# Optimization experiments

Measured on AMD Instinct MI355X. Metric: run time of the kernel, lower is better.

The kernel has to match this reference:

```python
import jax, jax.numpy as jnp
import numpy as np

P = 16          # patch size
NUM_HEADS = 8
WINDOW = 64     # window_size from SparseAttention(window_size=64)


def _layer_norm(x, w, b, eps=1e-5):
    mu = jnp.mean(x, axis=-1, keepdims=True)
    var = jnp.var(x, axis=-1, keepdims=True)
    return (x - mu) * jax.lax.rsqrt(var + eps) * w + b


def _sinusoidal_pe(num_patches, num_features, dtype):
    pos = jnp.arange(num_patches, dtype=jnp.float32)[:, None]            # [N,1]
    i = jnp.arange(0, num_features, 2, dtype=jnp.float32)                # [D/2]
    div = jnp.exp(-jnp.log(10000.0) * i / num_features)                  # [D/2]
    ang = pos * div                                                      # [N,D/2]
    pe = jnp.stack([jnp.sin(ang), jnp.cos(ang)], axis=-1).reshape(num_patches, num_features)
    return pe.astype(dtype)


def _ffn(x, w1, b1, w2, b2):
    # FeedForward: Linear -> GELU -> Linear (dropout inactive at eval)
    h = jax.nn.gelu(jnp.einsum('bnd,hd->bnh', x, w1) + b1)
    return jnp.einsum('bnh,dh->bnd', h, w2) + b2


def _windowed_attention(x, qkv_w, qkv_b, proj_w, proj_b):
    B, N, D = x.shape
    hd = D // NUM_HEADS
    qkv = jnp.einsum('bnd,ed->bne', x, qkv_w) + qkv_b                    # [B,N,3D]
    qkv = qkv.reshape(B, N, 3, NUM_HEADS, hd)
    q, k, v = qkv[:, :, 0], qkv[:, :, 1], qkv[:, :, 2]                   # [B,N,H,hd]
    nw = N // WINDOW
    # partition sequence into non-overlapping windows of 64 tokens
    q = q.reshape(B, nw, WINDOW, NUM_HEADS, hd).transpose(0, 3, 1, 2, 4)  # [B,H,nw,W,hd]
    k = k.reshape(B, nw, WINDOW, NUM_HEADS, hd).transpose(0, 3, 1, 2, 4)
    v = v.reshape(B, nw, WINDOW, NUM_HEADS, hd).transpose(0, 3, 1, 2, 4)
    scale = 1.0 / jnp.sqrt(jnp.asarray(hd, x.dtype))
    scores = jnp.einsum('bhwqd,bhwkd->bhwqk', q, k) * scale              # [B,H,nw,W,W]
    attn = jax.nn.softmax(scores, axis=-1)
    out = jnp.einsum('bhwqk,bhwkd->bhwqd', attn, v)                      # [B,H,nw,W,hd]
    out = out.transpose(0, 2, 3, 1, 4).reshape(B, N, D)
    return jnp.einsum('bnd,ed->bne', out, proj_w) + proj_b


def setup_inputs() -> dict:
    key = jax.random.key(0)
    ks = jax.random.split(key, 8)
    D, HF = 256, 1024
    s = lambda fan: 1.0 / np.sqrt(fan)
    return {
        'x': jax.random.normal(ks[0], (32, 3, 512, 512), jnp.float32),
        'conv_w': jax.random.normal(ks[1], (D, 3, P, P), jnp.float32) * s(3 * P * P),
        'conv_b': jnp.zeros((D,), jnp.float32),
        'ln_w': jnp.ones((D,), jnp.float32),
        'ln_b': jnp.zeros((D,), jnp.float32),
        'qkv_w': jax.random.normal(ks[2], (3 * D, D), jnp.float32) * s(D),
        'qkv_b': jnp.zeros((3 * D,), jnp.float32),
        'proj_w': jax.random.normal(ks[3], (D, D), jnp.float32) * s(D),
        'proj_b': jnp.zeros((D,), jnp.float32),
        'ff_w1': jax.random.normal(ks[4], (HF, D), jnp.float32) * s(D),
        'ff_b1': jnp.zeros((HF,), jnp.float32),
        'ff_w2': jax.random.normal(ks[5], (D, HF), jnp.float32) * s(HF),
        'ff_b2': jnp.zeros((D,), jnp.float32),
    }


def reference(x, conv_w, conv_b, ln_w, ln_b, qkv_w, qkv_b, proj_w, proj_b,
              ff_w1, ff_b1, ff_w2, ff_b2):
    B, C, H, W = x.shape
    D = conv_w.shape[0]
    # PatchEmbedding1: Conv2d(C, D, kernel=16, stride=16) == per-patch matmul, then LayerNorm
    nH, nW = H // P, W // P
    patches = x.reshape(B, C, nH, P, nW, P).transpose(0, 2, 4, 1, 3, 5).reshape(B, nH * nW, C * P * P)
    h = jnp.einsum('bnp,dp->bnd', patches, conv_w.reshape(D, -1)) + conv_b
    h = _layer_norm(h, ln_w, ln_b)
    # static sinusoidal position embedding
    h = h + _sinusoidal_pe(h.shape[1], D, h.dtype)
    # block 1: FFN -> sparse (windowed) attention -> residual
    identity = h
    h = _ffn(h, ff_w1, ff_b1, ff_w2, ff_b2)
    h = _windowed_attention(h, qkv_w, qkv_b, proj_w, proj_b)
    h = h + identity
    # block 2: shared FFN -> residual
    identity = h
    h = _ffn(h, ff_w1, ff_b1, ff_w2, ff_b2)
    return h + identity
```

## Files before the change

kernel.cpp:

```cpp
#include <hip/hip_runtime.h>
#include <math.h>


#define M_TOK 32768

typedef __attribute__((ext_vector_type(8))) short  short8;
typedef __attribute__((ext_vector_type(4))) float  f32x4;
typedef __attribute__((ext_vector_type(8))) unsigned short us8v;
typedef __attribute__((ext_vector_type(4))) unsigned short us4v;

__device__ __forceinline__ unsigned short f2b(float f) {
    union { float f; unsigned u; } c; c.f = f;
    unsigned r = c.u + 0x7fffu + ((c.u >> 16) & 1u);
    return (unsigned short)(r >> 16);
}
__device__ __forceinline__ float gelu_fast(float x) {
    const float c0 = 0.7978845608028654f;
    const float c1 = 0.044715f * 0.7978845608028654f;
    float z = x * (c0 + c1 * x * x);
    float e = __expf(-2.0f * z);
    return x * __builtin_amdgcn_rcpf(1.0f + e);
}
__device__ __forceinline__ void load_lds16(const unsigned short* g, void* lds) {
    __builtin_amdgcn_global_load_lds(
        (const __attribute__((address_space(1))) unsigned int*)g,
        (__attribute__((address_space(3))) unsigned int*)lds, 16, 0, 0);
}

__global__ __launch_bounds__(256) void cvt_f2b_kernel(
    const float* __restrict__ in, unsigned short* __restrict__ out, int n)
{
    int i = (blockIdx.x * 256 + threadIdx.x) * 4;
    if (i >= n) return;
    float4 v = *(const float4*)(in + i);
    us4v o;
    o[0] = f2b(v.x); o[1] = f2b(v.y); o[2] = f2b(v.z); o[3] = f2b(v.w);
    *(us4v*)(out + i) = o;
}

__global__ __launch_bounds__(256) void cvt_weights_kernel(
    const float* __restrict__ s0, const float* __restrict__ s1,
    const float* __restrict__ s2, const float* __restrict__ s3,
    const float* __restrict__ s4,
    unsigned short* __restrict__ d0, unsigned short* __restrict__ d1,
    unsigned short* __restrict__ d2, unsigned short* __restrict__ d3,
    unsigned short* __restrict__ d4)
{
    const int bid = blockIdx.x;
    const float* src; unsigned short* dst; int off;
    if      (bid < 192) { src = s0; dst = d0; off = bid; }
    else if (bid < 384) { src = s1; dst = d1; off = bid - 192; }
    else if (bid < 448) { src = s2; dst = d2; off = bid - 384; }
    else if (bid < 704) { src = s3; dst = d3; off = bid - 448; }
    else                { src = s4; dst = d4; off = bid - 704; }
    const int i = off * 1024 + threadIdx.x * 4;
    float4 v = *(const float4*)(src + i);
    us4v o;
    o[0] = f2b(v.x); o[1] = f2b(v.y); o[2] = f2b(v.z); o[3] = f2b(v.w);
    *(us4v*)(dst + i) = o;
}

__global__ __launch_bounds__(256) void pe_init_kernel(float* __restrict__ pe)
{
    const int pos = blockIdx.x;
    const int d   = threadIdx.x;
    const int ieven = d & ~1;
    float div = expf(-9.210340371976184f * (float)ieven * (1.0f / 256.0f));
    float ang = (float)pos * div;
    pe[pos * 256 + d] = (d & 1) ? cosf(ang) : sinf(ang);
}

template<bool GELU, bool RES, bool WF32, bool WB16>
__global__ __launch_bounds__(256) void mfma_gemm_kernel(
    const unsigned short* __restrict__ A, const unsigned short* __restrict__ W,
    const float* __restrict__ bias, const float* __restrict__ res,
    float* __restrict__ outF, unsigned short* __restrict__ outB,
    int M, int N, int K)
{
    __shared__ unsigned short As[128 * 64];
    __shared__ unsigned short Ws[128 * 64];

    const int t    = threadIdx.x;
    const int m0   = blockIdx.x * 128;
    const int n0   = blockIdx.y * 128;
    const int wv   = t >> 6, lane = t & 63;
    const int wr   = (wv >> 1) * 64, wc = (wv & 1) * 64;
    const int l15  = lane & 15, quad = lane >> 4;

    f32x4 acc[4][4];
#pragma unroll
    for (int i = 0; i < 4; i++)
#pragma unroll
        for (int j = 0; j < 4; j++)
#pragma unroll
            for (int r = 0; r < 4; r++) acc[i][j][r] = 0.0f;

    const int srow = wv * 8 + (lane >> 3);
    const int skk  = (((lane & 7) ^ ((lane >> 3) & 7)) * 8);
    const unsigned short* gA = A + (size_t)(m0 + srow) * K + skk;
    const unsigned short* gW = W + (size_t)(n0 + srow) * K + skk;
    char* lA = (char*)As + wv * 1024;
    char* lW = (char*)Ws + wv * 1024;

    const int cswz = (l15 & 7) * 8;

    for (int k0 = 0; k0 < K; k0 += 64) {
        __syncthreads();
#pragma unroll
        for (int s = 0; s < 4; s++) {
            load_lds16(gA + (size_t)(s * 32) * K + k0, lA + s * 4096);
            load_lds16(gW + (size_t)(s * 32) * K + k0, lW + s * 4096);
        }
        __syncthreads();

#pragma unroll
        for (int kh = 0; kh < 2; kh++) {
            const int coff = (kh * 32 + quad * 8) ^ cswz;
            short8 af[4], wf[4];
#pragma unroll
            for (int i = 0; i < 4; i++)
                af[i] = *(const short8*)&As[(wr + i * 16 + l15) * 64 + coff];
#pragma unroll
            for (int j = 0; j < 4; j++)
                wf[j] = *(const short8*)&Ws[(wc + j * 16 + l15) * 64 + coff];
#pragma unroll
            for (int i = 0; i < 4; i++)
#pragma unroll
                for (int j = 0; j < 4; j++)
                    acc[i][j] = __builtin_amdgcn_mfma_f32_16x16x32_bf16(
                        af[i], wf[j], acc[i][j], 0, 0, 0);
        }
    }

#pragma unroll
    for (int i = 0; i < 4; i++) {
        const int gr = m0 + wr + i * 16 + quad * 4;
#pragma unroll
        for (int j = 0; j < 4; j++) {
            const int gc = n0 + wc + j * 16 + l15;
            const float bv = bias[gc];
#pragma unroll
            for (int r = 0; r < 4; r++) {
                float v = acc[i][j][r] + bv;
                if (GELU) v = gelu_fast(v);
                if (RES)  v += res[(size_t)(gr + r) * N + gc];
                if (WF32) outF[(size_t)(gr + r) * N + gc] = v;
                if (WB16) outB[(size_t)(gr + r) * N + gc] = f2b(v);
            }
        }
    }
}

__global__ __launch_bounds__(256) void patch_mfma_kernel(
    const unsigned short* __restrict__ xb, const unsigned short* __restrict__ W,
    const float* __restrict__ bias, float* __restrict__ outF)
{
    __shared__ unsigned short As[128 * 64];
    __shared__ unsigned short Ws[128 * 64];

    const int t    = threadIdx.x;
    const int m0   = blockIdx.x * 128;
    const int n0   = blockIdx.y * 128;
    const int wv   = t >> 6, lane = t & 63;
    const int wr   = (wv >> 1) * 64, wc = (wv & 1) * 64;
    const int l15  = lane & 15, quad = lane >> 4;

    f32x4 acc[4][4];
#pragma unroll
    for (int i = 0; i < 4; i++)
#pragma unroll
        for (int j = 0; j < 4; j++)
#pragma unroll
            for (int r = 0; r < 4; r++) acc[i][j][r] = 0.0f;

    const int srow = wv * 8 + (lane >> 3);
    const int skk  = (((lane & 7) ^ ((lane >> 3) & 7)) * 8);
    size_t xoff[4];
#pragma unroll
    for (int s = 0; s < 4; s++) {
        const int m  = m0 + s * 32 + srow;
        const int b  = m >> 10;
        const int idx = m & 1023;
        const int hh = idx >> 5, ww = idx & 31;
        xoff[s] = ((size_t)(b * 3) * 512 + (size_t)(hh * 16)) * 512 + ww * 16;
    }
    const unsigned short* gW = W + (size_t)(n0 + srow) * 768 + skk;
    char* lA = (char*)As + wv * 1024;
    char* lW = (char*)Ws + wv * 1024;

    const int cswz = (l15 & 7) * 8;

    for (int k0 = 0; k0 < 768; k0 += 64) {
        const int k  = k0 + skk;
        const int c  = k >> 8;
        const int ph = (k >> 4) & 15;
        const int pw = k & 15;
        const size_t koff = (size_t)c * 262144 + (size_t)ph * 512 + pw;
        __syncthreads();
#pragma unroll
        for (int s = 0; s < 4; s++) {
            load_lds16(xb + xoff[s] + koff, lA + s * 4096);
            load_lds16(gW + (size_t)(s * 32) * 768 + k0, lW + s * 4096);
        }
        __syncthreads();

#pragma unroll
        for (int kh = 0; kh < 2; kh++) {
            const int coff = (kh * 32 + quad * 8) ^ cswz;
            short8 af[4], wf[4];
#pragma unroll
            for (int i = 0; i < 4; i++)
                af[i] = *(const short8*)&As[(wr + i * 16 + l15) * 64 + coff];
#pragma unroll
            for (int j = 0; j < 4; j++)
                wf[j] = *(const short8*)&Ws[(wc + j * 16 + l15) * 64 + coff];
#pragma unroll
            for (int i = 0; i < 4; i++)
#pragma unroll
                for (int j = 0; j < 4; j++)
                    acc[i][j] = __builtin_amdgcn_mfma_f32_16x16x32_bf16(
                        af[i], wf[j], acc[i][j], 0, 0, 0);
        }
    }

#pragma unroll
    for (int i = 0; i < 4; i++) {
        const int gr = m0 + wr + i * 16 + quad * 4;
#pragma unroll
        for (int j = 0; j < 4; j++) {
            const int gc = n0 + wc + j * 16 + l15;
            const float bv = bias[gc];
#pragma unroll
            for (int r = 0; r < 4; r++)
                outF[(size_t)(gr + r) * 256 + gc] = acc[i][j][r] + bv;
        }
    }
}

__global__ __launch_bounds__(256) void ln_pe_kernel(
    const float* __restrict__ in, const float* __restrict__ w,
    const float* __restrict__ b, const float* __restrict__ pe_t,
    float* __restrict__ outF, unsigned short* __restrict__ outB)
{
    const int m = blockIdx.x;
    const int d = threadIdx.x;
    float v = in[(size_t)m * 256 + d];

    float s = v, s2 = v * v;
#pragma unroll
    for (int off = 32; off > 0; off >>= 1) {
        s  += __shfl_down(s,  off, 64);
        s2 += __shfl_down(s2, off, 64);
    }
    __shared__ float ss[4], ss2[4], stats[2];
    const int lane = d & 63, wid = d >> 6;
    if (lane == 0) { ss[wid] = s; ss2[wid] = s2; }
    __syncthreads();
    if (d == 0) {
        float a  = ss[0] + ss[1] + ss[2] + ss[3];
        float a2 = ss2[0] + ss2[1] + ss2[2] + ss2[3];
        float mean = a * (1.0f / 256.0f);
        float var  = a2 * (1.0f / 256.0f) - mean * mean;
        stats[0] = mean;
        stats[1] = rsqrtf(var + 1e-5f);
    }
    __syncthreads();
    const float mean = stats[0], rstd = stats[1];

    const int pos = m & 1023;
    float pe = pe_t[pos * 256 + d];

    float o = (v - mean) * rstd * w[d] + b[d] + pe;
    outF[(size_t)m * 256 + d] = o;
    outB[(size_t)m * 256 + d] = f2b(o);
}

__global__ __launch_bounds__(256) void attn_mfma_kernel(
    const unsigned short* __restrict__ qkv, unsigned short* __restrict__ out)
{
    __shared__ unsigned short Ps[64 * 72];
    __shared__ unsigned short Vt[32 * 72];

    const int blk = blockIdx.x;
    const int h = blk & 7;
    const int w = (blk >> 3) & 15;
    const int b = blk >> 7;
    const int m_base = b * 1024 + w * 64;

    const int t = threadIdx.x;
    const int wv = t >> 6, lane = t & 63;
    const int l15 = lane & 15, quad = lane >> 4;

    {
        const int row = t >> 2;
        const int c0  = (t & 3) * 8;
        const unsigned short* src = qkv + (size_t)(m_base + row) * 768 + 512 + h * 32 + c0;
        us8v v = *(const us8v*)src;
#pragma unroll
        for (int j = 0; j < 8; j++) Vt[(c0 + j) * 72 + row] = v[j];
    }

    short8 aq = *(const short8*)(qkv + (size_t)(m_base + wv * 16 + l15) * 768 + h * 32 + quad * 8);
    f32x4 c[4];
#pragma unroll
    for (int j = 0; j < 4; j++) {
        short8 bk = *(const short8*)(qkv + (size_t)(m_base + j * 16 + l15) * 768 + 256 + h * 32 + quad * 8);
        f32x4 z = {0.0f, 0.0f, 0.0f, 0.0f};
        c[j] = __builtin_amdgcn_mfma_f32_16x16x32_bf16(aq, bk, z, 0, 0, 0);
    }

    const float scale = 0.17677669529663687f;
    float sm[4];
#pragma unroll
    for (int r = 0; r < 4; r++) {
        float m0 = -1e30f;
#pragma unroll
        for (int j = 0; j < 4; j++) { c[j][r] *= scale; m0 = fmaxf(m0, c[j][r]); }
#pragma unroll
        for (int d = 1; d < 16; d <<= 1) m0 = fmaxf(m0, __shfl_xor(m0, d, 64));
        float s0 = 0.0f;
#pragma unroll
        for (int j = 0; j < 4; j++) { float e = __expf(c[j][r] - m0); c[j][r] = e; s0 += e; }
#pragma unroll
        for (int d = 1; d < 16; d <<= 1) s0 += __shfl_xor(s0, d, 64);
        sm[r] = __builtin_amdgcn_rcpf(s0);
    }

#pragma unroll
    for (int r = 0; r < 4; r++) {
        const int prow = wv * 16 + quad * 4 + r;
#pragma unroll
        for (int j = 0; j < 4; j++)
            Ps[prow * 72 + j * 16 + l15] = f2b(c[j][r] * sm[r]);
    }
    __syncthreads();

    short8 ap0 = *(const short8*)&Ps[(wv * 16 + l15) * 72 + quad * 8];
    short8 ap1 = *(const short8*)&Ps[(wv * 16 + l15) * 72 + 32 + quad * 8];
    f32x4 o[2];
#pragma unroll
    for (int nt = 0; nt < 2; nt++) {
        short8 bv0 = *(const short8*)&Vt[(nt * 16 + l15) * 72 + quad * 8];
        short8 bv1 = *(const short8*)&Vt[(nt * 16 + l15) * 72 + 32 + quad * 8];
        f32x4 z = {0.0f, 0.0f, 0.0f, 0.0f};
        o[nt] = __builtin_amdgcn_mfma_f32_16x16x32_bf16(ap0, bv0, z, 0, 0, 0);
        o[nt] = __builtin_amdgcn_mfma_f32_16x16x32_bf16(ap1, bv1, o[nt], 0, 0, 0);
    }

#pragma unroll
    for (int nt = 0; nt < 2; nt++) {
#pragma unroll
        for (int r = 0; r < 4; r++) {
            const int row = m_base + wv * 16 + quad * 4 + r;
            out[(size_t)row * 256 + h * 32 + nt * 16 + l15] = f2b(o[nt][r]);
        }
    }
}

extern "C" void kernel_launch(void* const* d_in, const int* in_sizes, int n_in,
                              void* d_out, int out_size, void* d_ws, size_t ws_size,
                              hipStream_t stream)
{
    const float* x      = (const float*)d_in[0];
    const float* conv_w = (const float*)d_in[1];
    const float* conv_b = (const float*)d_in[2];
    const float* ln_w   = (const float*)d_in[3];
    const float* ln_b   = (const float*)d_in[4];
    const float* qkv_w  = (const float*)d_in[5];
    const float* qkv_b  = (const float*)d_in[6];
    const float* proj_w = (const float*)d_in[7];
    const float* proj_b = (const float*)d_in[8];
    const float* ff_w1  = (const float*)d_in[9];
    const float* ff_b1  = (const float*)d_in[10];
    const float* ff_w2  = (const float*)d_in[11];
    const float* ff_b2  = (const float*)d_in[12];
    float* out = (float*)d_out;

    char* ws = (char*)d_ws;
    unsigned short* xb    = (unsigned short*)(ws);
    unsigned short* hidb  = (unsigned short*)(ws);
    float*          h0    = (float*)(ws + 67108864);
    unsigned short* qkvb  = (unsigned short*)(ws + 67108864);
    float*          pe_t  = (float*)(ws + 100663296);
    float*          h1f   = (float*)(ws + 117440512);
    unsigned short* h1b   = (unsigned short*)(ws + 150994944);
    unsigned short* aob   = (unsigned short*)(ws + 150994944);
    unsigned short* f1b   = (unsigned short*)(ws + 167772160);
    unsigned short* h2b   = (unsigned short*)(ws + 167772160);
    unsigned short* wbase = (unsigned short*)(ws + 184549376);
    unsigned short* conv_wb = wbase;
    unsigned short* qkv_wb  = wbase + 196608;
    unsigned short* proj_wb = wbase + 393216;
    unsigned short* ff_w1b  = wbase + 458752;
    unsigned short* ff_w2b  = wbase + 720896;

    const int M = M_TOK;
    dim3 blk(256);

    cvt_f2b_kernel<<<dim3(25165824 / 1024), blk, 0, stream>>>(x, xb, 25165824);
    cvt_weights_kernel<<<dim3(960), blk, 0, stream>>>(
        conv_w, qkv_w, proj_w, ff_w1, ff_w2,
        conv_wb, qkv_wb, proj_wb, ff_w1b, ff_w2b);
    pe_init_kernel<<<dim3(1024), blk, 0, stream>>>(pe_t);

    patch_mfma_kernel<<<dim3(M / 128, 2), blk, 0, stream>>>(xb, conv_wb, conv_b, h0);
    ln_pe_kernel<<<dim3(M), blk, 0, stream>>>(h0, ln_w, ln_b, pe_t, h1f, h1b);
    mfma_gemm_kernel<true, false, false, true><<<dim3(M / 128, 8), blk, 0, stream>>>(
        h1b, ff_w1b, ff_b1, nullptr, nullptr, hidb, M, 1024, 256);
    mfma_gemm_kernel<false, false, false, true><<<dim3(M / 128, 2), blk, 0, stream>>>(
        hidb, ff_w2b, ff_b2, nullptr, nullptr, f1b, M, 256, 1024);
    mfma_gemm_kernel<false, false, false, true><<<dim3(M / 128, 6), blk, 0, stream>>>(
        f1b, qkv_wb, qkv_b, nullptr, nullptr, qkvb, M, 768, 256);
    attn_mfma_kernel<<<dim3(4096), blk, 0, stream>>>(qkvb, aob);
    mfma_gemm_kernel<false, true, true, true><<<dim3(M / 128, 2), blk, 0, stream>>>(
        aob, proj_wb, proj_b, h1f, out, h2b, M, 256, 256);
    mfma_gemm_kernel<true, false, false, true><<<dim3(M / 128, 8), blk, 0, stream>>>(
        h2b, ff_w1b, ff_b1, nullptr, nullptr, hidb, M, 1024, 256);
    mfma_gemm_kernel<false, true, true, false><<<dim3(M / 128, 2), blk, 0, stream>>>(
        hidb, ff_w2b, ff_b2, out, out, nullptr, M, 256, 1024);
}
```

Before: 418.0 us.

## Double-buffer LDS tiles in GEMM and patch-embed kernels to overlap loads with MFMA

Both MFMA GEMM kernels now keep two LDS stages for the A and W tiles. The next K-tile is issued through global_load_lds while the current one is consumed, with explicit vmcnt waits and s_barriers replacing the load-sync-compute-sync loop. The aim is to hide global memory latency behind the matrix math. LDS use per block doubles to 64 KB, which can lower occupancy. The unrolled-by-two loop assumes the K-tile count is even.

```diff
diff --git a/kernel.cpp b/kernel.cpp
--- a/kernel.cpp
+++ b/kernel.cpp
@@ -77,8 +77,8 @@
     float* __restrict__ outF, unsigned short* __restrict__ outB,
     int M, int N, int K)
 {
-    __shared__ unsigned short As[128 * 64];
-    __shared__ unsigned short Ws[128 * 64];
+    __shared__ unsigned short As[2 * 128 * 64];
+    __shared__ unsigned short Ws[2 * 128 * 64];
 
     const int t    = threadIdx.x;
     const int m0   = blockIdx.x * 128;
@@ -103,34 +103,60 @@
     char* lW = (char*)Ws + wv * 1024;
 
     const int cswz = (l15 & 7) * 8;
-
-    for (int k0 = 0; k0 < K; k0 += 64) {
-        __syncthreads();
-#pragma unroll
-        for (int s = 0; s < 4; s++) {
-            load_lds16(gA + (size_t)(s * 32) * K + k0, lA + s * 4096);
-            load_lds16(gW + (size_t)(s * 32) * K + k0, lW + s * 4096);
+    const int nt   = K >> 6;
+
+#define GSTAGE(tt, BUFOFF)                                                     \
+    {                                                                          \
+        const int kk = (tt) << 6;                                              \
+        _Pragma("unroll")                                                      \
+        for (int s = 0; s < 4; s++) {                                          \
+            load_lds16(gA + (size_t)(s * 32) * K + kk, lA + (BUFOFF) + s * 4096); \
+            load_lds16(gW + (size_t)(s * 32) * K + kk, lW + (BUFOFF) + s * 4096); \
+        }                                                                      \
+    }
+
+#define GCOMPUTE(Ab, Wb)                                                       \
+    {                                                                          \
+        _Pragma("unroll")                                                      \
+        for (int kh = 0; kh < 2; kh++) {                                       \
+            const int coff = (kh * 32 + quad * 8) ^ cswz;                      \
+            short8 af[4], wf[4];                                               \
+            _Pragma("unroll")                                                  \
+            for (int i = 0; i < 4; i++)                                        \
+                af[i] = *(const short8*)&(Ab)[(wr + i * 16 + l15) * 64 + coff];\
+            _Pragma("unroll")                                                  \
+            for (int j = 0; j < 4; j++)                                        \
+                wf[j] = *(const short8*)&(Wb)[(wc + j * 16 + l15) * 64 + coff];\
+            _Pragma("unroll")                                                  \
+            for (int i = 0; i < 4; i++)                                        \
+                _Pragma("unroll")                                              \
+                for (int j = 0; j < 4; j++)                                    \
+                    acc[i][j] = __builtin_amdgcn_mfma_f32_16x16x32_bf16(       \
+                        af[i], wf[j], acc[i][j], 0, 0, 0);                     \
+        }                                                                      \
+    }
+
+    GSTAGE(0, 0);
+    for (int tt = 0; tt < nt; tt += 2) {
+        GSTAGE(tt + 1, 16384);
+        asm volatile("s_waitcnt vmcnt(8)" ::: "memory");
+        __builtin_amdgcn_s_barrier();
+        __builtin_amdgcn_sched_barrier(0);
+        GCOMPUTE(As, Ws);
+        __builtin_amdgcn_s_barrier();
+        if (tt + 2 < nt) {
+            GSTAGE(tt + 2, 0);
+            asm volatile("s_waitcnt vmcnt(8)" ::: "memory");
+        } else {
+            asm volatile("s_waitcnt vmcnt(0)" ::: "memory");
         }
-        __syncthreads();
-
-#pragma unroll
-        for (int kh = 0; kh < 2; kh++) {
-            const int coff = (kh * 32 + quad * 8) ^ cswz;
-            short8 af[4], wf[4];
-#pragma unroll
-            for (int i = 0; i < 4; i++)
-                af[i] = *(const short8*)&As[(wr + i * 16 + l15) * 64 + coff];
-#pragma unroll
-            for (int j = 0; j < 4; j++)
-                wf[j] = *(const short8*)&Ws[(wc + j * 16 + l15) * 64 + coff];
-#pragma unroll
-            for (int i = 0; i < 4; i++)
-#pragma unroll
-                for (int j = 0; j < 4; j++)
-                    acc[i][j] = __builtin_amdgcn_mfma_f32_16x16x32_bf16(
-                        af[i], wf[j], acc[i][j], 0, 0, 0);
-        }
-    }
+        __builtin_amdgcn_s_barrier();
+        __builtin_amdgcn_sched_barrier(0);
+        GCOMPUTE(As + 8192, Ws + 8192);
+        __builtin_amdgcn_s_barrier();
+    }
+#undef GSTAGE
+#undef GCOMPUTE
 
 #pragma unroll
     for (int i = 0; i < 4; i++) {
@@ -155,8 +181,8 @@
     const unsigned short* __restrict__ xb, const unsigned short* __restrict__ W,
     const float* __restrict__ bias, float* __restrict__ outF)
 {
-    __shared__ unsigned short As[128 * 64];
-    __shared__ unsigned short Ws[128 * 64];
+    __shared__ unsigned short As[2 * 128 * 64];
+    __shared__ unsigned short Ws[2 * 128 * 64];
 
     const int t    = threadIdx.x;
     const int m0   = blockIdx.x * 128;
@@ -190,38 +216,63 @@
 
     const int cswz = (l15 & 7) * 8;
 
-    for (int k0 = 0; k0 < 768; k0 += 64) {
-        const int k  = k0 + skk;
-        const int c  = k >> 8;
-        const int ph = (k >> 4) & 15;
-        const int pw = k & 15;
-        const size_t koff = (size_t)c * 262144 + (size_t)ph * 512 + pw;
-        __syncthreads();
-#pragma unroll
-        for (int s = 0; s < 4; s++) {
-            load_lds16(xb + xoff[s] + koff, lA + s * 4096);
-            load_lds16(gW + (size_t)(s * 32) * 768 + k0, lW + s * 4096);
+#define PSTAGE(tt, BUFOFF)                                                     \
+    {                                                                          \
+        const int kk = ((tt) << 6) + skk;    \
+        const int c  = kk >> 8;                                                \
+        const int ph = (kk >> 4) & 15;                                         \
+        const int pw = kk & 15;                                                \
+        const size_t koff = (size_t)c * 262144 + (size_t)ph * 512 + pw;        \
+        _Pragma("unroll")                                                      \
+        for (int s = 0; s < 4; s++) {                                          \
+            load_lds16(xb + xoff[s] + koff, lA + (BUFOFF) + s * 4096);         \
+            load_lds16(gW + (size_t)(s * 32) * 768 + ((tt) << 6),              \
+                       lW + (BUFOFF) + s * 4096);                              \
+        }                                                                      \
+    }
+
+#define PCOMPUTE(Ab, Wb)                                                       \
+    {                                                                          \
+        _Pragma("unroll")                                                      \
+        for (int kh = 0; kh < 2; kh++) {                                       \
+            const int coff = (kh * 32 + quad * 8) ^ cswz;                      \
+            short8 af[4], wf[4];                                               \
+            _Pragma("unroll")                                                  \
+            for (int i = 0; i < 4; i++)                                        \
+                af[i] = *(const short8*)&(Ab)[(wr + i * 16 + l15) * 64 + coff];\
+            _Pragma("unroll")                                                  \
+            for (int j = 0; j < 4; j++)                                        \
+                wf[j] = *(const short8*)&(Wb)[(wc + j * 16 + l15) * 64 + coff];\
+            _Pragma("unroll")                                                  \
+            for (int i = 0; i < 4; i++)                                        \
+                _Pragma("unroll")                                              \
+                for (int j = 0; j < 4; j++)                                    \
+                    acc[i][j] = __builtin_amdgcn_mfma_f32_16x16x32_bf16(       \
+                        af[i], wf[j], acc[i][j], 0, 0, 0);                     \
+        }                                                                      \
+    }
+
+    PSTAGE(0, 0);
+    for (int tt = 0; tt < 12; tt += 2) {
+        PSTAGE(tt + 1, 16384);
+        asm volatile("s_waitcnt vmcnt(8)" ::: "memory");
+        __builtin_amdgcn_s_barrier();
+        __builtin_amdgcn_sched_barrier(0);
+        PCOMPUTE(As, Ws);
+        __builtin_amdgcn_s_barrier();
+        if (tt + 2 < 12) {
+            PSTAGE(tt + 2, 0);
+            asm volatile("s_waitcnt vmcnt(8)" ::: "memory");
+        } else {
+            asm volatile("s_waitcnt vmcnt(0)" ::: "memory");
         }
-        __syncthreads();
-
-#pragma unroll
-        for (int kh = 0; kh < 2; kh++) {
-            const int coff = (kh * 32 + quad * 8) ^ cswz;
-            short8 af[4], wf[4];
-#pragma unroll
-            for (int i = 0; i < 4; i++)
-                af[i] = *(const short8*)&As[(wr + i * 16 + l15) * 64 + coff];
-#pragma unroll
-            for (int j = 0; j < 4; j++)
-                wf[j] = *(const short8*)&Ws[(wc + j * 16 + l15) * 64 + coff];
-#pragma unroll
-            for (int i = 0; i < 4; i++)
-#pragma unroll
-                for (int j = 0; j < 4; j++)
-                    acc[i][j] = __builtin_amdgcn_mfma_f32_16x16x32_bf16(
-                        af[i], wf[j], acc[i][j], 0, 0, 0);
-        }
-    }
+        __builtin_amdgcn_s_barrier();
+        __builtin_amdgcn_sched_barrier(0);
+        PCOMPUTE(As + 8192, Ws + 8192);
+        __builtin_amdgcn_s_barrier();
+    }
+#undef PSTAGE
+#undef PCOMPUTE
 
 #pragma unroll
     for (int i = 0; i < 4; i++) {
```

Measured after the change: 406.0 us. -2.9%, faster.

## Load GEMM fragments directly from global memory with register double-buffering, swap MFMA operands

Applied to the files above, without the earlier changes.

Both MFMA GEMM kernels drop the LDS staging and the per-step block barriers. Each wave now reads its A and W fragments straight from global memory into registers, double-buffered across k-steps so loads overlap MFMAs. The MFMA operands are swapped (W first), so each lane holds four consecutive output columns, which allows vectorized float4/ushort4 bias, residual and output stores. The cost is that data reuse across waves now depends on the L1/L2 caches instead of shared memory, so global traffic and load latency exposure per wave go up.

```diff
diff --git a/kernel.cpp b/kernel.cpp
--- a/kernel.cpp
+++ b/kernel.cpp
@@ -20,11 +20,6 @@
     float z = x * (c0 + c1 * x * x);
     float e = __expf(-2.0f * z);
     return x * __builtin_amdgcn_rcpf(1.0f + e);
-}
-__device__ __forceinline__ void load_lds16(const unsigned short* g, void* lds) {
-    __builtin_amdgcn_global_load_lds(
-        (const __attribute__((address_space(1))) unsigned int*)g,
-        (__attribute__((address_space(3))) unsigned int*)lds, 16, 0, 0);
 }
 
 __global__ __launch_bounds__(256) void cvt_f2b_kernel(
@@ -77,9 +72,6 @@
     float* __restrict__ outF, unsigned short* __restrict__ outB,
     int M, int N, int K)
 {
-    __shared__ unsigned short As[128 * 64];
-    __shared__ unsigned short Ws[128 * 64];
-
     const int t    = threadIdx.x;
     const int m0   = blockIdx.x * 128;
     const int n0   = blockIdx.y * 128;
@@ -89,63 +81,75 @@
 
     f32x4 acc[4][4];
 #pragma unroll
+    for (int j = 0; j < 4; j++)
+#pragma unroll
+        for (int i = 0; i < 4; i++)
+#pragma unroll
+            for (int r = 0; r < 4; r++) acc[j][i][r] = 0.0f;
+
+    const unsigned short* pA[4];
+    const unsigned short* pW[4];
+#pragma unroll
     for (int i = 0; i < 4; i++)
-#pragma unroll
-        for (int j = 0; j < 4; j++)
-#pragma unroll
-            for (int r = 0; r < 4; r++) acc[i][j][r] = 0.0f;
-
-    const int srow = wv * 8 + (lane >> 3);
-    const int skk  = (((lane & 7) ^ ((lane >> 3) & 7)) * 8);
-    const unsigned short* gA = A + (size_t)(m0 + srow) * K + skk;
-    const unsigned short* gW = W + (size_t)(n0 + srow) * K + skk;
-    char* lA = (char*)As + wv * 1024;
-    char* lW = (char*)Ws + wv * 1024;
-
-    const int cswz = (l15 & 7) * 8;
-
-    for (int k0 = 0; k0 < K; k0 += 64) {
-        __syncthreads();
-#pragma unroll
-        for (int s = 0; s < 4; s++) {
-            load_lds16(gA + (size_t)(s * 32) * K + k0, lA + s * 4096);
-            load_lds16(gW + (size_t)(s * 32) * K + k0, lW + s * 4096);
-        }
-        __syncthreads();
-
-#pragma unroll
-        for (int kh = 0; kh < 2; kh++) {
-            const int coff = (kh * 32 + quad * 8) ^ cswz;
-            short8 af[4], wf[4];
-#pragma unroll
-            for (int i = 0; i < 4; i++)
-                af[i] = *(const short8*)&As[(wr + i * 16 + l15) * 64 + coff];
-#pragma unroll
-            for (int j = 0; j < 4; j++)
-                wf[j] = *(const short8*)&Ws[(wc + j * 16 + l15) * 64 + coff];
-#pragma unroll
-            for (int i = 0; i < 4; i++)
-#pragma unroll
-                for (int j = 0; j < 4; j++)
-                    acc[i][j] = __builtin_amdgcn_mfma_f32_16x16x32_bf16(
-                        af[i], wf[j], acc[i][j], 0, 0, 0);
-        }
-    }
-
-#pragma unroll
-    for (int i = 0; i < 4; i++) {
-        const int gr = m0 + wr + i * 16 + quad * 4;
-#pragma unroll
-        for (int j = 0; j < 4; j++) {
-            const int gc = n0 + wc + j * 16 + l15;
-            const float bv = bias[gc];
+        pA[i] = A + (size_t)(m0 + wr + i * 16 + l15) * K + quad * 8;
+#pragma unroll
+    for (int j = 0; j < 4; j++)
+        pW[j] = W + (size_t)(n0 + wc + j * 16 + l15) * K + quad * 8;
+
+#define LOADF(AF, WF, kc)                                                      \
+    {                                                                          \
+        _Pragma("unroll")                                                      \
+        for (int i = 0; i < 4; i++) AF[i] = *(const short8*)(pA[i] + (kc) * 32); \
+        _Pragma("unroll")                                                      \
+        for (int j = 0; j < 4; j++) WF[j] = *(const short8*)(pW[j] + (kc) * 32); \
+    }
+#define MF(AF, WF)                                                             \
+    {                                                                          \
+        _Pragma("unroll")                                                      \
+        for (int j = 0; j < 4; j++)                                            \
+            _Pragma("unroll")                                                  \
+            for (int i = 0; i < 4; i++)                                        \
+                acc[j][i] = __builtin_amdgcn_mfma_f32_16x16x32_bf16(           \
+                    WF[j], AF[i], acc[j][i], 0, 0, 0);                         \
+    }
+
+    const int ks = K >> 5;
+    short8 a0[4], w0[4], a1[4], w1[4];
+    LOADF(a0, w0, 0);
+    for (int kc = 0; kc < ks; kc += 2) {
+        LOADF(a1, w1, kc + 1);
+        MF(a0, w0);
+        if (kc + 2 < ks) LOADF(a0, w0, kc + 2);
+        MF(a1, w1);
+    }
+#undef LOADF
+#undef MF
+
+#pragma unroll
+    for (int j = 0; j < 4; j++) {
+        const int nb = n0 + wc + j * 16 + quad * 4;
+        const f32x4 bv = *(const f32x4*)(bias + nb);
+#pragma unroll
+        for (int i = 0; i < 4; i++) {
+            const size_t row = (size_t)(m0 + wr + i * 16 + l15) * N + nb;
+            f32x4 v;
 #pragma unroll
             for (int r = 0; r < 4; r++) {
-                float v = acc[i][j][r] + bv;
-                if (GELU) v = gelu_fast(v);
-                if (RES)  v += res[(size_t)(gr + r) * N + gc];
-                if (WF32) outF[(size_t)(gr + r) * N + gc] = v;
-                if (WB16) outB[(size_t)(gr + r) * N + gc] = f2b(v);
+                float x = acc[j][i][r] + bv[r];
+                if (GELU) x = gelu_fast(x);
+                v[r] = x;
+            }
+            if (RES) {
+                const f32x4 rr = *(const f32x4*)(res + row);
+#pragma unroll
+                for (int r = 0; r < 4; r++) v[r] += rr[r];
+            }
+            if (WF32) *(f32x4*)(outF + row) = v;
+            if (WB16) {
+                us4v o;
+#pragma unroll
+                for (int r = 0; r < 4; r++) o[r] = f2b(v[r]);
+                *(us4v*)(outB + row) = o;
             }
         }
     }
@@ -155,9 +159,6 @@
     const unsigned short* __restrict__ xb, const unsigned short* __restrict__ W,
     const float* __restrict__ bias, float* __restrict__ outF)
 {
-    __shared__ unsigned short As[128 * 64];
-    __shared__ unsigned short Ws[128 * 64];
-
     const int t    = threadIdx.x;
     const int m0   = blockIdx.x * 128;
     const int n0   = blockIdx.y * 128;
@@ -167,72 +168,70 @@
 
     f32x4 acc[4][4];
 #pragma unroll
-    for (int i = 0; i < 4; i++)
-#pragma unroll
-        for (int j = 0; j < 4; j++)
-#pragma unroll
-            for (int r = 0; r < 4; r++) acc[i][j][r] = 0.0f;
-
-    const int srow = wv * 8 + (lane >> 3);
-    const int skk  = (((lane & 7) ^ ((lane >> 3) & 7)) * 8);
-    size_t xoff[4];
-#pragma unroll
-    for (int s = 0; s < 4; s++) {
-        const int m  = m0 + s * 32 + srow;
-        const int b  = m >> 10;
+    for (int j = 0; j < 4; j++)
+#pragma unroll
+        for (int i = 0; i < 4; i++)
+#pragma unroll
+            for (int r = 0; r < 4; r++) acc[j][i][r] = 0.0f;
+
+    size_t xoffP[4];
+#pragma unroll
+    for (int i = 0; i < 4; i++) {
+        const int m   = m0 + wr + i * 16 + l15;
+        const int b   = m >> 10;
         const int idx = m & 1023;
-        const int hh = idx >> 5, ww = idx & 31;
-        xoff[s] = ((size_t)(b * 3) * 512 + (size_t)(hh * 16)) * 512 + ww * 16;
-    }
-    const unsigned short* gW = W + (size_t)(n0 + srow) * 768 + skk;
-    char* lA = (char*)As + wv * 1024;
-    char* lW = (char*)Ws + wv * 1024;
-
-    const int cswz = (l15 & 7) * 8;
-
-    for (int k0 = 0; k0 < 768; k0 += 64) {
-        const int k  = k0 + skk;
-        const int c  = k >> 8;
-        const int ph = (k >> 4) & 15;
-        const int pw = k & 15;
-        const size_t koff = (size_t)c * 262144 + (size_t)ph * 512 + pw;
-        __syncthreads();
-#pragma unroll
-        for (int s = 0; s < 4; s++) {
-            load_lds16(xb + xoff[s] + koff, lA + s * 4096);
-            load_lds16(gW + (size_t)(s * 32) * 768 + k0, lW + s * 4096);
-        }
-        __syncthreads();
-
-#pragma unroll
-        for (int kh = 0; kh < 2; kh++) {
-            const int coff = (kh * 32 + quad * 8) ^ cswz;
-            short8 af[4], wf[4];
-#pragma unroll
-            for (int i = 0; i < 4; i++)
-                af[i] = *(const short8*)&As[(wr + i * 16 + l15) * 64 + coff];
-#pragma unroll
-            for (int j = 0; j < 4; j++)
-                wf[j] = *(const short8*)&Ws[(wc + j * 16 + l15) * 64 + coff];
-#pragma unroll
-            for (int i = 0; i < 4; i++)
-#pragma unroll
-                for (int j = 0; j < 4; j++)
-                    acc[i][j] = __builtin_amdgcn_mfma_f32_16x16x32_bf16(
-                        af[i], wf[j], acc[i][j], 0, 0, 0);
-        }
-    }
-
-#pragma unroll
-    for (int i = 0; i < 4; i++) {
-        const int gr = m0 + wr + i * 16 + quad * 4;
-#pragma unroll
-        for (int j = 0; j < 4; j++) {
-            const int gc = n0 + wc + j * 16 + l15;
-            const float bv = bias[gc];
-#pragma unroll
-            for (int r = 0; r < 4; r++)
-                outF[(size_t)(gr + r) * 256 + gc] = acc[i][j][r] + bv;
+        const int hh  = idx >> 5, ww = idx & 31;
+        xoffP[i] = (size_t)b * 786432 + (size_t)hh * 8192 + ww * 16;
+    }
+    const unsigned short* pW[4];
+#pragma unroll
+    for (int j = 0; j < 4; j++)
+        pW[j] = W + (size_t)(n0 + wc + j * 16 + l15) * 768 + quad * 8;
+
+#define PLOADF(AF, WF, kc)                                                     \
+    {                                                                          \
+        const int k  = (kc) * 32 + quad * 8;                                   \
+        const int c  = k >> 8;                                                 \
+        const int ph = (k >> 4) & 15;                                          \
+        const int pw = k & 15;                                                 \
+        const size_t koff = (size_t)c * 262144 + (size_t)ph * 512 + pw;        \
+        _Pragma("unroll")                                                      \
+        for (int i = 0; i < 4; i++) AF[i] = *(const short8*)(xb + xoffP[i] + koff); \
+        _Pragma("unroll")                                                      \
+        for (int j = 0; j < 4; j++) WF[j] = *(const short8*)(pW[j] + (kc) * 32); \
+    }
+#define PMF(AF, WF)                                                            \
+    {                                                                          \
+        _Pragma("unroll")                                                      \
+        for (int j = 0; j < 4; j++)                                            \
+            _Pragma("unroll")                                                  \
+            for (int i = 0; i < 4; i++)                                        \
+                acc[j][i] = __builtin_amdgcn_mfma_f32_16x16x32_bf16(           \
+                    WF[j], AF[i], acc[j][i], 0, 0, 0);                         \
+    }
+
+    short8 a0[4], w0[4], a1[4], w1[4];
+    PLOADF(a0, w0, 0);
+    for (int kc = 0; kc < 24; kc += 2) {
+        PLOADF(a1, w1, kc + 1);
+        PMF(a0, w0);
+        if (kc + 2 < 24) PLOADF(a0, w0, kc + 2);
+        PMF(a1, w1);
+    }
+#undef PLOADF
+#undef PMF
+
+#pragma unroll
+    for (int j = 0; j < 4; j++) {
+        const int nb = n0 + wc + j * 16 + quad * 4;
+        const f32x4 bv = *(const f32x4*)(bias + nb);
+#pragma unroll
+        for (int i = 0; i < 4; i++) {
+            const size_t row = (size_t)(m0 + wr + i * 16 + l15) * 256 + nb;
+            f32x4 v;
+#pragma unroll
+            for (int r = 0; r < 4; r++) v[r] = acc[j][i][r] + bv[r];
+            *(f32x4*)(outF + row) = v;
         }
     }
 }
```

After: 620.0 us. 1.48x slower.
